# Performance work log

Measured on AMD Instinct MI355X. Metric: run time of the kernel, lower is better.

The kernel has to match this reference:

```python
import jax, jax.numpy as jnp
import numpy as np

N_SRC, N_DST, E = 50000, 50000, 800000
D_GT, D_AG = 64, 64
HID, HEADS = 256, 4
FPH = HID // HEADS  # 64
N_ACT = 16
NEG_SLOPE = 0.2  # DGL GATv2Conv default negative_slope


def setup_inputs() -> dict:
    key = jax.random.key(0)
    ks = jax.random.split(key, 16)
    f32 = jnp.float32
    return {
        "feat_gt": jax.random.normal(ks[0], (N_SRC, D_GT), f32),
        "feat_agent": jax.random.normal(ks[1], (N_DST, D_AG), f32),
        "h0": jax.random.normal(ks[2], (N_DST, HID), f32),
        "edge_src": jax.random.randint(ks[3], (E,), 0, N_SRC),
        "edge_dst": jax.random.randint(ks[4], (E,), 0, N_DST),
        "W_src": jax.random.normal(ks[5], (D_GT, HID), f32) * 0.1,
        "b_src": jnp.zeros((HID,), f32),
        "W_dst": jax.random.normal(ks[6], (D_AG, HID), f32) * 0.1,
        "b_dst": jnp.zeros((HID,), f32),
        "attn": jax.random.normal(ks[7], (HEADS, FPH), f32) * 0.1,
        "W_res": jax.random.normal(ks[8], (D_AG, HID), f32) * 0.1,
        "b_res": jnp.zeros((HID,), f32),
        "W_ih": jax.random.normal(ks[9], (3 * HID, HID), f32) * 0.05,
        "W_hh": jax.random.normal(ks[10], (3 * HID, HID), f32) * 0.05,
        "b_ih": jnp.zeros((3 * HID,), f32),
        "b_hh": jnp.zeros((3 * HID,), f32),
        "W_out": jax.random.normal(ks[11], (HID, N_ACT), f32) * 0.05,
        "b_out": jnp.zeros((N_ACT,), f32),
    }


def _gatv2(feat_gt, feat_agent, edge_src, edge_dst,
           W_src, b_src, W_dst, b_dst, attn, W_res, b_res):
    # GATv2Conv (bipartite, share_weights=False, residual=True, activation=ReLU)
    fs = (feat_gt @ W_src + b_src).reshape(N_SRC, HEADS, FPH)    # [Ns,H,F]
    fd = (feat_agent @ W_dst + b_dst).reshape(N_DST, HEADS, FPH)  # [Nd,H,F]
    e = fs[edge_src] + fd[edge_dst]                               # [E,H,F]
    e = jnp.where(e > 0, e, NEG_SLOPE * e)                        # LeakyReLU
    score = jnp.einsum('ehf,hf->eh', e, attn)                     # [E,H]
    # edge softmax segmented by destination node
    smax = jax.lax.stop_gradient(
        jax.ops.segment_max(score, edge_dst, num_segments=N_DST))  # [Nd,H]
    ex = jnp.exp(score - smax[edge_dst])
    den = jax.ops.segment_sum(ex, edge_dst, num_segments=N_DST)   # [Nd,H]
    alpha = ex / den[edge_dst]                                    # [E,H]
    msg = alpha[:, :, None] * fs[edge_src]                        # [E,H,F]
    rst = jax.ops.segment_sum(msg, edge_dst, num_segments=N_DST)  # [Nd,H,F]
    rst = rst.reshape(N_DST, HID) + (feat_agent @ W_res + b_res)  # residual
    return jax.nn.relu(rst)


def _gru_cell(x, h, W_ih, W_hh, b_ih, b_hh):
    gi = x @ W_ih.T + b_ih
    gh = h @ W_hh.T + b_hh
    ir, iz, inn = jnp.split(gi, 3, axis=-1)
    hr, hz, hn = jnp.split(gh, 3, axis=-1)
    r = jax.nn.sigmoid(ir + hr)
    z = jax.nn.sigmoid(iz + hz)
    n = jnp.tanh(inn + r * hn)
    return (1.0 - z) * n + z * h


def reference(feat_gt, feat_agent, h0, edge_src, edge_dst,
              W_src, b_src, W_dst, b_dst, attn, W_res, b_res,
              W_ih, W_hh, b_ih, b_hh, W_out, b_out):
    x = _gatv2(feat_gt, feat_agent, edge_src, edge_dst,
               W_src, b_src, W_dst, b_dst, attn, W_res, b_res)  # [Nd,HID]
    h = _gru_cell(x, h0, W_ih, W_hh, b_ih, b_hh)                # [Nd,HID]
    logits = h @ W_out + b_out                                  # [Nd,N_ACT]
    return (logits, h)
```

## Files before the change

kernel.cpp:

```cpp
#include <hip/hip_runtime.h>
#include <stdint.h>

#define N_SRCN 50000
#define N_DSTN 50000
#define NE     800000
#define HIDN   256
#define NEG    0.2f

typedef __attribute__((ext_vector_type(8)))  short short8;
typedef __attribute__((ext_vector_type(16))) float float16v;

__device__ __forceinline__ float bf2f(unsigned short u){
    union { unsigned u32; float f; } c; c.u32 = ((unsigned)u) << 16; return c.f;
}
__device__ __forceinline__ unsigned short f2bf(float f){
    union { float f; unsigned u; } c; c.f = f;
    unsigned r = c.u + 0x7fffu + ((c.u >> 16) & 1u);
    return (unsigned short)(r >> 16);
}
__device__ __forceinline__ float4 ld4b(const unsigned short* p){
    uint2 u = *reinterpret_cast<const uint2*>(p);
    float4 r;
    r.x = bf2f((unsigned short)(u.x & 0xffff));
    r.y = bf2f((unsigned short)(u.x >> 16));
    r.z = bf2f((unsigned short)(u.y & 0xffff));
    r.w = bf2f((unsigned short)(u.y >> 16));
    return r;
}

__global__ void pack_kernel(const float* __restrict__ Wsrc, const float* __restrict__ Wdst,
                            const float* __restrict__ Wres, const float* __restrict__ Wih,
                            const float* __restrict__ Whh,
                            unsigned short* __restrict__ Wt2,
                            unsigned short* __restrict__ Wf){
    int i = blockIdx.x * 256 + threadIdx.x;
    if (i < 49152){
        int which = i >> 14, j = i & 16383;
        int k = j >> 8, c = j & 255;
        const float* W = (which == 0) ? Wsrc : (which == 1 ? Wdst : Wres);
        float v = W[j];
        int off = which * 16384 + (c >> 5) * 2048 + (k >> 4) * 512
                + (((k >> 3) & 1) * 32 + (c & 31)) * 8 + (k & 7);
        Wt2[off] = f2bf(v);
    } else if (i < 49152 + 196608){
        int o = i - 49152;
        int row = o >> 8, k = o & 255;
        int g = row >> 8, c = row & 255;
        float v = Wih[o];
        int off = g * 131072 + (c >> 5) * 16384 + (k >> 4) * 512
                + (((k >> 3) & 1) * 32 + (c & 31)) * 8 + (k & 7);
        Wf[off] = f2bf(v);
    } else if (i < 49152 + 393216){
        int o = i - 49152 - 196608;
        int row = o >> 8, k = o & 255;
        int g = row >> 8, c = row & 255;
        float v = Whh[o];
        int off = g * 131072 + (c >> 5) * 16384 + (16 + (k >> 4)) * 512
                + (((k >> 3) & 1) * 32 + (c & 31)) * 8 + (k & 7);
        Wf[off] = f2bf(v);
    }
}

__global__ __launch_bounds__(256) void proj_kernel(
        const float* __restrict__ Agt, const float* __restrict__ Aag,
        const unsigned short* __restrict__ Wt2,
        const float* __restrict__ bsrc, const float* __restrict__ bdst,
        const float* __restrict__ bres,
        unsigned short* __restrict__ fs, unsigned short* __restrict__ fd,
        unsigned short* __restrict__ resb){
    __shared__ unsigned short As[64 * 72];
    __shared__ unsigned short Cs[64 * 72];
    int z = blockIdx.z;
    const float* A = (z == 0) ? Agt : Aag;
    const float* bias = (z == 0) ? bsrc : (z == 1 ? bdst : bres);
    unsigned short* out = (z == 0) ? fs : (z == 1 ? fd : resb);
    const unsigned short* Wb = Wt2 + z * 16384;
    int tid = threadIdx.x;
    int m0 = blockIdx.y * 64;
    #pragma unroll
    for (int i = 0; i < 4; ++i){
        int ci = tid + i * 256;
        int row = ci >> 4;
        int k4 = (ci & 15) << 2;
        int gr = m0 + row; if (gr >= N_SRCN) gr = N_SRCN - 1;
        float4 v = *reinterpret_cast<const float4*>(A + (size_t)gr * 64 + k4);
        unsigned short* dp = As + row * 72 + k4;
        dp[0] = f2bf(v.x); dp[1] = f2bf(v.y); dp[2] = f2bf(v.z); dp[3] = f2bf(v.w);
    }
    __syncthreads();
    int lane = tid & 63, w = tid >> 6;
    int l31 = lane & 31, half = lane >> 5;
    int msub = (w & 1) * 32;
    int cbw = blockIdx.x * 2 + (w >> 1);
    const unsigned short* bb = Wb + cbw * 2048 + lane * 8;
    const unsigned short* ap = As + (msub + l31) * 72 + half * 8;
    float16v acc = {0,0,0,0,0,0,0,0,0,0,0,0,0,0,0,0};
    #pragma unroll
    for (int ks = 0; ks < 4; ++ks){
        short8 a = *reinterpret_cast<const short8*>(ap + ks * 16);
        short8 b = *reinterpret_cast<const short8*>(bb + ks * 512);
        acc = __builtin_amdgcn_mfma_f32_32x32x16_bf16(a, b, acc, 0, 0, 0);
    }
    float bv = bias[cbw * 32 + l31];
    int ccol = (w >> 1) * 32 + l31;
    #pragma unroll
    for (int r = 0; r < 16; ++r){
        int row = (r & 3) + 8 * (r >> 2) + 4 * half + msub;
        Cs[row * 72 + ccol] = f2bf(acc[r] + bv);
    }
    __syncthreads();
    int srow = tid >> 2, chunk = tid & 3;
    int gr2 = m0 + srow;
    if (gr2 < N_SRCN){
        const uint4* sp = reinterpret_cast<const uint4*>(Cs + srow * 72 + chunk * 16);
        uint4* gp = reinterpret_cast<uint4*>(out + (size_t)gr2 * 256 + blockIdx.x * 64 + chunk * 16);
        gp[0] = sp[0];
        gp[1] = sp[1];
    }
}

__global__ void degree_kernel(const int* __restrict__ dst, int* __restrict__ deg){
    int i = blockIdx.x * 256 + threadIdx.x;
    if (i < NE) atomicAdd(&deg[dst[i]], 1);
}

__global__ void scan1_kernel(const int* __restrict__ deg, int* __restrict__ bsum){
    __shared__ int s[256];
    int tid = threadIdx.x;
    int i = blockIdx.x * 256 + tid;
    s[tid] = (i < N_DSTN) ? deg[i] : 0;
    __syncthreads();
    #pragma unroll
    for (int off = 128; off; off >>= 1){
        if (tid < off) s[tid] += s[tid + off];
        __syncthreads();
    }
    if (tid == 0) bsum[blockIdx.x] = s[0];
}

__global__ void scan2_kernel(const int* __restrict__ bsum, int* __restrict__ boff){
    __shared__ int s[256];
    int tid = threadIdx.x;
    int v = (tid < 196) ? bsum[tid] : 0;
    s[tid] = v;
    __syncthreads();
    #pragma unroll
    for (int off = 1; off < 256; off <<= 1){
        int t = (tid >= off) ? s[tid - off] : 0;
        __syncthreads();
        s[tid] += t;
        __syncthreads();
    }
    if (tid < 196) boff[tid] = s[tid] - v;
}

__global__ void scan3_kernel(const int* __restrict__ deg, const int* __restrict__ boff,
                             int* __restrict__ ptr, int* __restrict__ cursor){
    __shared__ int s[256];
    int tid = threadIdx.x;
    int i = blockIdx.x * 256 + tid;
    int v = (i < N_DSTN) ? deg[i] : 0;
    s[tid] = v;
    __syncthreads();
    #pragma unroll
    for (int off = 1; off < 256; off <<= 1){
        int t = (tid >= off) ? s[tid - off] : 0;
        __syncthreads();
        s[tid] += t;
        __syncthreads();
    }
    int ex = s[tid] - v + boff[blockIdx.x];
    if (i < N_DSTN){ ptr[i] = ex; cursor[i] = ex; }
}

__global__ void scatter_kernel(const int* __restrict__ src, const int* __restrict__ dst,
                               int* __restrict__ cursor, int* __restrict__ csr){
    int i = blockIdx.x * 256 + threadIdx.x;
    if (i < NE){
        int d = dst[i];
        int pos = atomicAdd(&cursor[d], 1);
        csr[pos] = src[i];
    }
}

__global__ __launch_bounds__(256) void aggregate_kernel(
        const unsigned short* __restrict__ fs, const unsigned short* __restrict__ fd,
        const unsigned short* __restrict__ res, const float* __restrict__ attn,
        const int* __restrict__ ptr, const int* __restrict__ deg,
        const int* __restrict__ csr, unsigned short* __restrict__ x){
    int wv = threadIdx.x >> 6;
    int d = blockIdx.x * 4 + wv;
    if (d >= N_DSTN) return;
    int lane = threadIdx.x & 63;
    int c4 = lane * 4;
    float4 fdv = ld4b(fd + (size_t)d * 256 + c4);
    float4 at = *reinterpret_cast<const float4*>(attn + (lane >> 4) * 64 + (lane & 15) * 4);
    int p = ptr[d], dg = deg[d];
    float l = 0.f;
    float4 acc = make_float4(0.f, 0.f, 0.f, 0.f);
    for (int base = 0; base < dg; base += 64){
        int cnt = min(64, dg - base);
        int sreg = (lane < cnt) ? csr[p + base + lane] : 0;
        float4 b0 = ld4b(fs + (size_t)__shfl(sreg, 0) * 256 + c4);
        float4 b1 = ld4b(fs + (size_t)__shfl(sreg, 1 & 63) * 256 + c4);
        float4 b2 = ld4b(fs + (size_t)__shfl(sreg, 2 & 63) * 256 + c4);
        float4 b3 = ld4b(fs + (size_t)__shfl(sreg, 3 & 63) * 256 + c4);
        for (int j = 0; j < cnt; j += 4){
            float4 n0 = ld4b(fs + (size_t)__shfl(sreg, (j + 4) & 63) * 256 + c4);
            float4 n1 = ld4b(fs + (size_t)__shfl(sreg, (j + 5) & 63) * 256 + c4);
            float4 n2 = ld4b(fs + (size_t)__shfl(sreg, (j + 6) & 63) * 256 + c4);
            float4 n3 = ld4b(fs + (size_t)__shfl(sreg, (j + 7) & 63) * 256 + c4);
#define PROC(BV, T) { \
            float ex = BV.x + fdv.x; ex = ex > 0.f ? ex : NEG * ex; \
            float ey = BV.y + fdv.y; ey = ey > 0.f ? ey : NEG * ey; \
            float ez = BV.z + fdv.z; ez = ez > 0.f ? ez : NEG * ez; \
            float ew = BV.w + fdv.w; ew = ew > 0.f ? ew : NEG * ew; \
            float part = ex * at.x + ey * at.y + ez * at.z + ew * at.w; \
            part += __shfl_xor(part, 1); \
            part += __shfl_xor(part, 2); \
            part += __shfl_xor(part, 4); \
            part += __shfl_xor(part, 8); \
            float wgt = ((j + (T)) < cnt) ? __expf(part) : 0.f; \
            l += wgt; \
            acc.x = fmaf(wgt, BV.x, acc.x); \
            acc.y = fmaf(wgt, BV.y, acc.y); \
            acc.z = fmaf(wgt, BV.z, acc.z); \
            acc.w = fmaf(wgt, BV.w, acc.w); }
            PROC(b0, 0) PROC(b1, 1) PROC(b2, 2) PROC(b3, 3)
#undef PROC
            b0 = n0; b1 = n1; b2 = n2; b3 = n3;
        }
    }
    float inv = (l > 0.f) ? 1.f / l : 0.f;
    float4 rv = ld4b(res + (size_t)d * 256 + c4);
    float xx = fmaxf(fmaf(acc.x, inv, rv.x), 0.f);
    float xy = fmaxf(fmaf(acc.y, inv, rv.y), 0.f);
    float xz = fmaxf(fmaf(acc.z, inv, rv.z), 0.f);
    float xw = fmaxf(fmaf(acc.w, inv, rv.w), 0.f);
    uint2 o;
    o.x = (unsigned)f2bf(xx) | ((unsigned)f2bf(xy) << 16);
    o.y = (unsigned)f2bf(xz) | ((unsigned)f2bf(xw) << 16);
    *reinterpret_cast<uint2*>(x + (size_t)d * 256 + c4) = o;
}

__global__ __launch_bounds__(256, 4) void gru_kernel(
        const unsigned short* __restrict__ Xb,
        const float* __restrict__ H0, const unsigned short* __restrict__ Wf,
        const float* __restrict__ bih, const float* __restrict__ bhh,
        float* __restrict__ outH){
    __shared__ unsigned short As[128 * 136];
    int tid = threadIdx.x;
    int sid = blockIdx.x;
    int xcd = sid & 7, rr_ = sid >> 3;
    int strip = xcd * 49 + (rr_ >> 3);
    int cb = rr_ & 7;
    int m0 = strip << 7;
    int w = tid >> 6, lane = tid & 63;
    int l31 = lane & 31, half = lane >> 5;
    int cg = cb * 32 + l31;
    const unsigned short* bb = Wf + cb * 16384 + lane * 8;
    float16v ar  = {0,0,0,0,0,0,0,0,0,0,0,0,0,0,0,0};
    float16v az = ar, anx = ar, anh = ar;
    #pragma unroll
    for (int kc = 0; kc < 512; kc += 128){
        __syncthreads();
        if (kc < 256){
            #pragma unroll
            for (int i = 0; i < 8; ++i){
                int ci = tid + i * 256;
                int row = ci >> 4;
                int k8 = (ci & 15) << 3;
                int gr = m0 + row; if (gr >= N_DSTN) gr = N_DSTN - 1;
                *reinterpret_cast<uint4*>(As + row * 136 + k8) =
                    *reinterpret_cast<const uint4*>(Xb + (size_t)gr * 256 + kc + k8);
            }
        } else {
            #pragma unroll
            for (int i = 0; i < 8; ++i){
                int ci = tid + i * 256;
                int row = ci >> 4;
                int k8 = (ci & 15) << 3;
                int gr = m0 + row; if (gr >= N_DSTN) gr = N_DSTN - 1;
                const float* hp = H0 + (size_t)gr * 256 + (kc - 256) + k8;
                float4 f0 = *reinterpret_cast<const float4*>(hp);
                float4 f1 = *reinterpret_cast<const float4*>(hp + 4);
                uint4 o;
                o.x = (unsigned)f2bf(f0.x) | ((unsigned)f2bf(f0.y) << 16);
                o.y = (unsigned)f2bf(f0.z) | ((unsigned)f2bf(f0.w) << 16);
                o.z = (unsigned)f2bf(f1.x) | ((unsigned)f2bf(f1.y) << 16);
                o.w = (unsigned)f2bf(f1.z) | ((unsigned)f2bf(f1.w) << 16);
                *reinterpret_cast<uint4*>(As + row * 136 + k8) = o;
            }
        }
        __syncthreads();
        const unsigned short* ap = As + (w * 32 + l31) * 136 + half * 8;
        #pragma unroll
        for (int ks = 0; ks < 8; ++ks){
            int kk = (kc >> 4) + ks;
            short8 a  = *reinterpret_cast<const short8*>(ap + ks * 16);
            short8 br = *reinterpret_cast<const short8*>(bb + (size_t)kk * 512);
            short8 bz = *reinterpret_cast<const short8*>(bb + 131072 + (size_t)kk * 512);
            short8 bn = *reinterpret_cast<const short8*>(bb + 262144 + (size_t)kk * 512);
            ar = __builtin_amdgcn_mfma_f32_32x32x16_bf16(a, br, ar, 0, 0, 0);
            az = __builtin_amdgcn_mfma_f32_32x32x16_bf16(a, bz, az, 0, 0, 0);
            if (kc < 256) anx = __builtin_amdgcn_mfma_f32_32x32x16_bf16(a, bn, anx, 0, 0, 0);
            else          anh = __builtin_amdgcn_mfma_f32_32x32x16_bf16(a, bn, anh, 0, 0, 0);
        }
    }
    float rb = bih[cg] + bhh[cg];
    float zb = bih[256 + cg] + bhh[256 + cg];
    float bin = bih[512 + cg], bhn = bhh[512 + cg];
    #pragma unroll
    for (int r = 0; r < 16; ++r){
        int m = m0 + w * 32 + (r & 3) + 8 * (r >> 2) + 4 * half;
        if (m < N_DSTN){
            float h0v = H0[(size_t)m * 256 + cg];
            float rrg = 1.f / (1.f + __expf(-(ar[r] + rb)));
            float zz = 1.f / (1.f + __expf(-(az[r] + zb)));
            float nx = anx[r] + bin + rrg * (anh[r] + bhn);
            float tm = __expf(-2.f * fabsf(nx));
            float nn = (1.f - tm) / (1.f + tm);
            nn = (nx >= 0.f) ? nn : -nn;
            outH[(size_t)m * 256 + cg] = (1.f - zz) * nn + zz * h0v;
        }
    }
}

__global__ __launch_bounds__(256) void logits_kernel(
        const float* __restrict__ H, const float* __restrict__ Wout,
        const float* __restrict__ bout, float* __restrict__ outL){
    __shared__ float Hl[16 * 260];
    __shared__ float Wl[16 * 260];
    int tid = threadIdx.x;
    int m0 = blockIdx.x * 16;
    #pragma unroll
    for (int i = 0; i < 4; ++i){
        int ci = tid + i * 256;
        int row = ci >> 6;
        int c4 = (ci & 63) << 2;
        int gr = m0 + row; if (gr >= N_DSTN) gr = N_DSTN - 1;
        float4 v = *reinterpret_cast<const float4*>(H + (size_t)gr * 256 + c4);
        float* dp = Hl + row * 260 + c4;
        dp[0] = v.x; dp[1] = v.y; dp[2] = v.z; dp[3] = v.w;
    }
    #pragma unroll
    for (int i = 0; i < 16; ++i){
        int ci = tid + i * 256;
        int c = ci >> 4, j = ci & 15;
        Wl[j * 260 + c] = Wout[c * 16 + j];
    }
    __syncthreads();
    int row = tid >> 4, j = tid & 15;
    const float* hr = Hl + row * 260;
    const float* wr = Wl + j * 260;
    float acc = bout[j];
    #pragma unroll
    for (int c = 0; c < 256; c += 4){
        float4 hv = *reinterpret_cast<const float4*>(hr + c);
        float4 wv = *reinterpret_cast<const float4*>(wr + c);
        acc = fmaf(hv.x, wv.x, fmaf(hv.y, wv.y, fmaf(hv.z, wv.z, fmaf(hv.w, wv.w, acc))));
    }
    int m = m0 + row;
    if (m < N_DSTN) outL[m * 16 + j] = acc;
}

extern "C" void kernel_launch(void* const* d_in, const int* in_sizes, int n_in,
                              void* d_out, int out_size, void* d_ws, size_t ws_size,
                              hipStream_t stream){
    const float* feat_gt = (const float*)d_in[0];
    const float* feat_ag = (const float*)d_in[1];
    const float* h0      = (const float*)d_in[2];
    const int*   e_src   = (const int*)d_in[3];
    const int*   e_dst   = (const int*)d_in[4];
    const float* W_src   = (const float*)d_in[5];
    const float* b_src   = (const float*)d_in[6];
    const float* W_dst   = (const float*)d_in[7];
    const float* b_dst   = (const float*)d_in[8];
    const float* attn    = (const float*)d_in[9];
    const float* W_res   = (const float*)d_in[10];
    const float* b_res   = (const float*)d_in[11];
    const float* W_ih    = (const float*)d_in[12];
    const float* W_hh    = (const float*)d_in[13];
    const float* b_ih    = (const float*)d_in[14];
    const float* b_hh    = (const float*)d_in[15];
    const float* W_out   = (const float*)d_in[16];
    const float* b_out   = (const float*)d_in[17];

    float* outL = (float*)d_out;
    float* outH = outL + (size_t)N_DSTN * 16;

    char* ws = (char*)d_ws;
    size_t off = 0;
    auto alloc = [&](size_t bytes) -> void* {
        void* p = ws + off; off = (off + bytes + 255) & ~(size_t)255; return p;
    };
    unsigned short* fs   = (unsigned short*)alloc((size_t)N_SRCN * 256 * 2);
    unsigned short* fd   = (unsigned short*)alloc((size_t)N_DSTN * 256 * 2);
    unsigned short* res  = (unsigned short*)alloc((size_t)N_DSTN * 256 * 2);
    unsigned short* xb   = (unsigned short*)alloc((size_t)N_DSTN * 256 * 2);
    unsigned short* Wt2  = (unsigned short*)alloc(49152 * 2);
    unsigned short* Wf   = (unsigned short*)alloc(393216 * 2);
    int* deg    = (int*)alloc(N_DSTN * 4);
    int* ptr    = (int*)alloc(N_DSTN * 4);
    int* cursor = (int*)alloc(N_DSTN * 4);
    int* csr    = (int*)alloc((size_t)NE * 4);
    int* bsum   = (int*)alloc(256 * 4);
    int* boff   = (int*)alloc(256 * 4);

    hipMemsetAsync(deg, 0, N_DSTN * 4, stream);
    pack_kernel<<<1728, 256, 0, stream>>>(W_src, W_dst, W_res, W_ih, W_hh, Wt2, Wf);

    proj_kernel<<<dim3(4, 782, 3), 256, 0, stream>>>(feat_gt, feat_ag, Wt2,
                                                     b_src, b_dst, b_res, fs, fd, res);

    degree_kernel<<<3125, 256, 0, stream>>>(e_dst, deg);
    scan1_kernel<<<196, 256, 0, stream>>>(deg, bsum);
    scan2_kernel<<<1, 256, 0, stream>>>(bsum, boff);
    scan3_kernel<<<196, 256, 0, stream>>>(deg, boff, ptr, cursor);
    scatter_kernel<<<3125, 256, 0, stream>>>(e_src, e_dst, cursor, csr);
    aggregate_kernel<<<12500, 256, 0, stream>>>(fs, fd, res, attn, ptr, deg, csr, xb);

    gru_kernel<<<3136, 256, 0, stream>>>(xb, h0, Wf, b_ih, b_hh, outH);
    logits_kernel<<<3125, 256, 0, stream>>>(outH, W_out, b_out, outL);
}
```

Baseline: 485.2 us.

## Deepen aggregate gather prefetch, double-buffer GRU GEMM, split logits accumulators

The aggregate kernel now prefetches 8 neighbor rows per step instead of 4, giving more memory-level parallelism on the gather. The GRU kernel is restructured so each block covers 64 output columns with two 32-row MFMA tiles per wave. It also double-buffers its A tiles in LDS with register prefetch of the next 64-wide K chunk, which halves the grid and cuts syncs per chunk. The logits dot product uses four independent accumulators to shorten the FMA dependency chain. The changes raise register pressure in the aggregate and GRU kernels, and the GRU launch bound drops to 2 blocks per SIMD, which lowers occupancy.

After: 489.2 us. Within noise of the previous version (+0.8%).

```diff
diff --git a/kernel.cpp b/kernel.cpp
--- a/kernel.cpp
+++ b/kernel.cpp
@@ -17,6 +17,9 @@
     union { float f; unsigned u; } c; c.f = f;
     unsigned r = c.u + 0x7fffu + ((c.u >> 16) & 1u);
     return (unsigned short)(r >> 16);
+}
+__device__ __forceinline__ unsigned pack2(float a, float b){
+    return (unsigned)f2bf(a) | ((unsigned)f2bf(b) << 16);
 }
 __device__ __forceinline__ float4 ld4b(const unsigned short* p){
     uint2 u = *reinterpret_cast<const uint2*>(p);
@@ -201,34 +204,36 @@
     for (int base = 0; base < dg; base += 64){
         int cnt = min(64, dg - base);
         int sreg = (lane < cnt) ? csr[p + base + lane] : 0;
-        float4 b0 = ld4b(fs + (size_t)__shfl(sreg, 0) * 256 + c4);
-        float4 b1 = ld4b(fs + (size_t)__shfl(sreg, 1 & 63) * 256 + c4);
-        float4 b2 = ld4b(fs + (size_t)__shfl(sreg, 2 & 63) * 256 + c4);
-        float4 b3 = ld4b(fs + (size_t)__shfl(sreg, 3 & 63) * 256 + c4);
-        for (int j = 0; j < cnt; j += 4){
-            float4 n0 = ld4b(fs + (size_t)__shfl(sreg, (j + 4) & 63) * 256 + c4);
-            float4 n1 = ld4b(fs + (size_t)__shfl(sreg, (j + 5) & 63) * 256 + c4);
-            float4 n2 = ld4b(fs + (size_t)__shfl(sreg, (j + 6) & 63) * 256 + c4);
-            float4 n3 = ld4b(fs + (size_t)__shfl(sreg, (j + 7) & 63) * 256 + c4);
-#define PROC(BV, T) { \
-            float ex = BV.x + fdv.x; ex = ex > 0.f ? ex : NEG * ex; \
-            float ey = BV.y + fdv.y; ey = ey > 0.f ? ey : NEG * ey; \
-            float ez = BV.z + fdv.z; ez = ez > 0.f ? ez : NEG * ez; \
-            float ew = BV.w + fdv.w; ew = ew > 0.f ? ew : NEG * ew; \
-            float part = ex * at.x + ey * at.y + ez * at.z + ew * at.w; \
-            part += __shfl_xor(part, 1); \
-            part += __shfl_xor(part, 2); \
-            part += __shfl_xor(part, 4); \
-            part += __shfl_xor(part, 8); \
-            float wgt = ((j + (T)) < cnt) ? __expf(part) : 0.f; \
-            l += wgt; \
-            acc.x = fmaf(wgt, BV.x, acc.x); \
-            acc.y = fmaf(wgt, BV.y, acc.y); \
-            acc.z = fmaf(wgt, BV.z, acc.z); \
-            acc.w = fmaf(wgt, BV.w, acc.w); }
-            PROC(b0, 0) PROC(b1, 1) PROC(b2, 2) PROC(b3, 3)
-#undef PROC
-            b0 = n0; b1 = n1; b2 = n2; b3 = n3;
+        float4 buf[8];
+        #pragma unroll
+        for (int t = 0; t < 8; ++t)
+            buf[t] = ld4b(fs + (size_t)__shfl(sreg, t & 63) * 256 + c4);
+        for (int j = 0; j < cnt; j += 8){
+            float4 nbuf[8];
+            #pragma unroll
+            for (int t = 0; t < 8; ++t)
+                nbuf[t] = ld4b(fs + (size_t)__shfl(sreg, (j + 8 + t) & 63) * 256 + c4);
+            #pragma unroll
+            for (int t = 0; t < 8; ++t){
+                float4 bv = buf[t];
+                float ex = bv.x + fdv.x; ex = ex > 0.f ? ex : NEG * ex;
+                float ey = bv.y + fdv.y; ey = ey > 0.f ? ey : NEG * ey;
+                float ez = bv.z + fdv.z; ez = ez > 0.f ? ez : NEG * ez;
+                float ew = bv.w + fdv.w; ew = ew > 0.f ? ew : NEG * ew;
+                float part = ex * at.x + ey * at.y + ez * at.z + ew * at.w;
+                part += __shfl_xor(part, 1);
+                part += __shfl_xor(part, 2);
+                part += __shfl_xor(part, 4);
+                part += __shfl_xor(part, 8);
+                float wgt = ((j + t) < cnt) ? __expf(part) : 0.f;
+                l += wgt;
+                acc.x = fmaf(wgt, bv.x, acc.x);
+                acc.y = fmaf(wgt, bv.y, acc.y);
+                acc.z = fmaf(wgt, bv.z, acc.z);
+                acc.w = fmaf(wgt, bv.w, acc.w);
+            }
+            #pragma unroll
+            for (int t = 0; t < 8; ++t) buf[t] = nbuf[t];
         }
     }
     float inv = (l > 0.f) ? 1.f / l : 0.f;
@@ -238,92 +243,126 @@
     float xz = fmaxf(fmaf(acc.z, inv, rv.z), 0.f);
     float xw = fmaxf(fmaf(acc.w, inv, rv.w), 0.f);
     uint2 o;
-    o.x = (unsigned)f2bf(xx) | ((unsigned)f2bf(xy) << 16);
-    o.y = (unsigned)f2bf(xz) | ((unsigned)f2bf(xw) << 16);
+    o.x = pack2(xx, xy);
+    o.y = pack2(xz, xw);
     *reinterpret_cast<uint2*>(x + (size_t)d * 256 + c4) = o;
 }
 
-__global__ __launch_bounds__(256, 4) void gru_kernel(
+__global__ __launch_bounds__(256, 2) void gru_kernel(
         const unsigned short* __restrict__ Xb,
         const float* __restrict__ H0, const unsigned short* __restrict__ Wf,
         const float* __restrict__ bih, const float* __restrict__ bhh,
         float* __restrict__ outH){
-    __shared__ unsigned short As[128 * 136];
+    __shared__ unsigned short As[2][128 * 72];
     int tid = threadIdx.x;
     int sid = blockIdx.x;
-    int xcd = sid & 7, rr_ = sid >> 3;
-    int strip = xcd * 49 + (rr_ >> 3);
-    int cb = rr_ & 7;
+    int xcd = sid & 7, r_ = sid >> 3;
+    int strip = xcd * 49 + (r_ >> 2);
+    int cbp = r_ & 3;
     int m0 = strip << 7;
     int w = tid >> 6, lane = tid & 63;
     int l31 = lane & 31, half = lane >> 5;
+    int whalf = w & 1;
+    int cb = cbp * 2 + (w >> 1);
     int cg = cb * 32 + l31;
-    const unsigned short* bb = Wf + cb * 16384 + lane * 8;
-    float16v ar  = {0,0,0,0,0,0,0,0,0,0,0,0,0,0,0,0};
-    float16v az = ar, anx = ar, anh = ar;
-    #pragma unroll
-    for (int kc = 0; kc < 512; kc += 128){
-        __syncthreads();
-        if (kc < 256){
-            #pragma unroll
-            for (int i = 0; i < 8; ++i){
-                int ci = tid + i * 256;
-                int row = ci >> 4;
-                int k8 = (ci & 15) << 3;
-                int gr = m0 + row; if (gr >= N_DSTN) gr = N_DSTN - 1;
-                *reinterpret_cast<uint4*>(As + row * 136 + k8) =
-                    *reinterpret_cast<const uint4*>(Xb + (size_t)gr * 256 + kc + k8);
-            }
-        } else {
-            #pragma unroll
-            for (int i = 0; i < 8; ++i){
-                int ci = tid + i * 256;
-                int row = ci >> 4;
-                int k8 = (ci & 15) << 3;
-                int gr = m0 + row; if (gr >= N_DSTN) gr = N_DSTN - 1;
-                const float* hp = H0 + (size_t)gr * 256 + (kc - 256) + k8;
-                float4 f0 = *reinterpret_cast<const float4*>(hp);
-                float4 f1 = *reinterpret_cast<const float4*>(hp + 4);
-                uint4 o;
-                o.x = (unsigned)f2bf(f0.x) | ((unsigned)f2bf(f0.y) << 16);
-                o.y = (unsigned)f2bf(f0.z) | ((unsigned)f2bf(f0.w) << 16);
-                o.z = (unsigned)f2bf(f1.x) | ((unsigned)f2bf(f1.y) << 16);
-                o.w = (unsigned)f2bf(f1.z) | ((unsigned)f2bf(f1.w) << 16);
-                *reinterpret_cast<uint4*>(As + row * 136 + k8) = o;
+    const unsigned short* bb = Wf + (size_t)cb * 16384 + lane * 8;
+
+    int srow[4], sk8[4], sgr[4];
+    #pragma unroll
+    for (int i = 0; i < 4; ++i){
+        int ci = tid + i * 256;
+        srow[i] = ci >> 3;
+        sk8[i]  = (ci & 7) << 3;
+        int gr = m0 + srow[i]; if (gr >= N_DSTN) gr = N_DSTN - 1;
+        sgr[i] = gr;
+    }
+
+    float16v ar0 = {0,0,0,0,0,0,0,0,0,0,0,0,0,0,0,0};
+    float16v ar1 = ar0, az0 = ar0, az1 = ar0;
+    float16v anx0 = ar0, anx1 = ar0, anh0 = ar0, anh1 = ar0;
+
+    uint4 pf[4];
+    #pragma unroll
+    for (int i = 0; i < 4; ++i)
+        pf[i] = *reinterpret_cast<const uint4*>(Xb + (size_t)sgr[i] * 256 + sk8[i]);
+    #pragma unroll
+    for (int i = 0; i < 4; ++i)
+        *reinterpret_cast<uint4*>(&As[0][srow[i] * 72 + sk8[i]]) = pf[i];
+    __syncthreads();
+
+    for (int c = 0; c < 8; ++c){
+        uint4 npf[4];
+        if (c < 7){
+            int cn = c + 1;
+            if (cn < 4){
+                #pragma unroll
+                for (int i = 0; i < 4; ++i)
+                    npf[i] = *reinterpret_cast<const uint4*>(
+                        Xb + (size_t)sgr[i] * 256 + cn * 64 + sk8[i]);
+            } else {
+                #pragma unroll
+                for (int i = 0; i < 4; ++i){
+                    const float* hp = H0 + (size_t)sgr[i] * 256 + (cn - 4) * 64 + sk8[i];
+                    float4 f0 = *reinterpret_cast<const float4*>(hp);
+                    float4 f1 = *reinterpret_cast<const float4*>(hp + 4);
+                    npf[i].x = pack2(f0.x, f0.y);
+                    npf[i].y = pack2(f0.z, f0.w);
+                    npf[i].z = pack2(f1.x, f1.y);
+                    npf[i].w = pack2(f1.z, f1.w);
+                }
             }
         }
-        __syncthreads();
-        const unsigned short* ap = As + (w * 32 + l31) * 136 + half * 8;
+        const unsigned short* ap = As[c & 1] + (whalf * 64 + l31) * 72 + half * 8;
         #pragma unroll
-        for (int ks = 0; ks < 8; ++ks){
-            int kk = (kc >> 4) + ks;
-            short8 a  = *reinterpret_cast<const short8*>(ap + ks * 16);
+        for (int ks = 0; ks < 4; ++ks){
+            int kk = c * 4 + ks;
+            short8 a0 = *reinterpret_cast<const short8*>(ap + ks * 16);
+            short8 a1 = *reinterpret_cast<const short8*>(ap + 32 * 72 + ks * 16);
             short8 br = *reinterpret_cast<const short8*>(bb + (size_t)kk * 512);
             short8 bz = *reinterpret_cast<const short8*>(bb + 131072 + (size_t)kk * 512);
             short8 bn = *reinterpret_cast<const short8*>(bb + 262144 + (size_t)kk * 512);
-            ar = __builtin_amdgcn_mfma_f32_32x32x16_bf16(a, br, ar, 0, 0, 0);
-            az = __builtin_amdgcn_mfma_f32_32x32x16_bf16(a, bz, az, 0, 0, 0);
-            if (kc < 256) anx = __builtin_amdgcn_mfma_f32_32x32x16_bf16(a, bn, anx, 0, 0, 0);
-            else          anh = __builtin_amdgcn_mfma_f32_32x32x16_bf16(a, bn, anh, 0, 0, 0);
+            ar0 = __builtin_amdgcn_mfma_f32_32x32x16_bf16(a0, br, ar0, 0, 0, 0);
+            ar1 = __builtin_amdgcn_mfma_f32_32x32x16_bf16(a1, br, ar1, 0, 0, 0);
+            az0 = __builtin_amdgcn_mfma_f32_32x32x16_bf16(a0, bz, az0, 0, 0, 0);
+            az1 = __builtin_amdgcn_mfma_f32_32x32x16_bf16(a1, bz, az1, 0, 0, 0);
+            if (c < 4){
+                anx0 = __builtin_amdgcn_mfma_f32_32x32x16_bf16(a0, bn, anx0, 0, 0, 0);
+                anx1 = __builtin_amdgcn_mfma_f32_32x32x16_bf16(a1, bn, anx1, 0, 0, 0);
+            } else {
+                anh0 = __builtin_amdgcn_mfma_f32_32x32x16_bf16(a0, bn, anh0, 0, 0, 0);
+                anh1 = __builtin_amdgcn_mfma_f32_32x32x16_bf16(a1, bn, anh1, 0, 0, 0);
+            }
         }
-    }
+        if (c < 7){
+            #pragma unroll
+            for (int i = 0; i < 4; ++i)
+                *reinterpret_cast<uint4*>(&As[(c + 1) & 1][srow[i] * 72 + sk8[i]]) = npf[i];
+        }
+        __syncthreads();
+    }
+
     float rb = bih[cg] + bhh[cg];
     float zb = bih[256 + cg] + bhh[256 + cg];
     float bin = bih[512 + cg], bhn = bhh[512 + cg];
-    #pragma unroll
-    for (int r = 0; r < 16; ++r){
-        int m = m0 + w * 32 + (r & 3) + 8 * (r >> 2) + 4 * half;
-        if (m < N_DSTN){
-            float h0v = H0[(size_t)m * 256 + cg];
-            float rrg = 1.f / (1.f + __expf(-(ar[r] + rb)));
-            float zz = 1.f / (1.f + __expf(-(az[r] + zb)));
-            float nx = anx[r] + bin + rrg * (anh[r] + bhn);
-            float tm = __expf(-2.f * fabsf(nx));
-            float nn = (1.f - tm) / (1.f + tm);
-            nn = (nx >= 0.f) ? nn : -nn;
-            outH[(size_t)m * 256 + cg] = (1.f - zz) * nn + zz * h0v;
-        }
-    }
+    int mbase = m0 + whalf * 64;
+#define GRU_EPI(VR, VZ, VNX, VNH, MSOFF)                                        \
+    _Pragma("unroll")                                                           \
+    for (int r = 0; r < 16; ++r){                                               \
+        int m = mbase + (MSOFF) + (r & 3) + 8 * (r >> 2) + 4 * half;            \
+        if (m < N_DSTN){                                                        \
+            float h0v = H0[(size_t)m * 256 + cg];                               \
+            float rr = 1.f / (1.f + __expf(-((VR)[r] + rb)));                   \
+            float zz = 1.f / (1.f + __expf(-((VZ)[r] + zb)));                   \
+            float nx = (VNX)[r] + bin + rr * ((VNH)[r] + bhn);                  \
+            float tm = __expf(-2.f * fabsf(nx));                                \
+            float nn = (1.f - tm) / (1.f + tm);                                 \
+            nn = (nx >= 0.f) ? nn : -nn;                                        \
+            outH[(size_t)m * 256 + cg] = (1.f - zz) * nn + zz * h0v;            \
+        }                                                                       \
+    }
+    GRU_EPI(ar0, az0, anx0, anh0, 0)
+    GRU_EPI(ar1, az1, anx1, anh1, 32)
+#undef GRU_EPI
 }
 
 __global__ __launch_bounds__(256) void logits_kernel(
@@ -353,15 +392,24 @@
     int row = tid >> 4, j = tid & 15;
     const float* hr = Hl + row * 260;
     const float* wr = Wl + j * 260;
-    float acc = bout[j];
-    #pragma unroll
-    for (int c = 0; c < 256; c += 4){
-        float4 hv = *reinterpret_cast<const float4*>(hr + c);
-        float4 wv = *reinterpret_cast<const float4*>(wr + c);
-        acc = fmaf(hv.x, wv.x, fmaf(hv.y, wv.y, fmaf(hv.z, wv.z, fmaf(hv.w, wv.w, acc))));
+    float a0 = bout[j], a1 = 0.f, a2 = 0.f, a3 = 0.f;
+    #pragma unroll
+    for (int c = 0; c < 256; c += 16){
+        float4 h0v = *reinterpret_cast<const float4*>(hr + c);
+        float4 w0v = *reinterpret_cast<const float4*>(wr + c);
+        float4 h1v = *reinterpret_cast<const float4*>(hr + c + 4);
+        float4 w1v = *reinterpret_cast<const float4*>(wr + c + 4);
+        float4 h2v = *reinterpret_cast<const float4*>(hr + c + 8);
+        float4 w2v = *reinterpret_cast<const float4*>(wr + c + 8);
+        float4 h3v = *reinterpret_cast<const float4*>(hr + c + 12);
+        float4 w3v = *reinterpret_cast<const float4*>(wr + c + 12);
+        a0 = fmaf(h0v.x, w0v.x, fmaf(h0v.y, w0v.y, fmaf(h0v.z, w0v.z, fmaf(h0v.w, w0v.w, a0))));
+        a1 = fmaf(h1v.x, w1v.x, fmaf(h1v.y, w1v.y, fmaf(h1v.z, w1v.z, fmaf(h1v.w, w1v.w, a1))));
+        a2 = fmaf(h2v.x, w2v.x, fmaf(h2v.y, w2v.y, fmaf(h2v.z, w2v.z, fmaf(h2v.w, w2v.w, a2))));
+        a3 = fmaf(h3v.x, w3v.x, fmaf(h3v.y, w3v.y, fmaf(h3v.z, w3v.z, fmaf(h3v.w, w3v.w, a3))));
     }
     int m = m0 + row;
-    if (m < N_DSTN) outL[m * 16 + j] = acc;
+    if (m < N_DSTN) outL[m * 16 + j] = (a0 + a1) + (a2 + a3);
 }
 
 extern "C" void kernel_launch(void* const* d_in, const int* in_sizes, int n_in,
@@ -420,6 +468,6 @@
     scatter_kernel<<<3125, 256, 0, stream>>>(e_src, e_dst, cursor, csr);
     aggregate_kernel<<<12500, 256, 0, stream>>>(fs, fd, res, attn, ptr, deg, csr, xb);
 
-    gru_kernel<<<3136, 256, 0, stream>>>(xb, h0, Wf, b_ih, b_hh, outH);
+    gru_kernel<<<1568, 256, 0, stream>>>(xb, h0, Wf, b_ih, b_hh, outH);
     logits_kernel<<<3125, 256, 0, stream>>>(outH, W_out, b_out, outL);
 }
```
